# Performance work log

Hardware: AMD Instinct MI355X
Metric: run time of the kernel (lower is better)

## Reference

```python
import jax, jax.numpy as jnp
import numpy as np

B, S, D = 4, 1024, 1024
H = 16
DK = D // H  # per-head dim_q = dim_k = 64
DFF = 4096
EPS = 1e-5


def _layer_norm(x, g, b):
    m = jnp.mean(x, axis=-1, keepdims=True)
    v = jnp.mean((x - m) ** 2, axis=-1, keepdims=True)
    return (x - m) / jnp.sqrt(v + EPS) * g + b


def setup_inputs() -> dict:
    key = jax.random.key(0)
    ks = jax.random.split(key, 16)
    sd = 1.0 / np.sqrt(D)
    sk = 1.0 / np.sqrt(H * DK)
    sf = 1.0 / np.sqrt(DFF)
    return {
        "src": jax.random.normal(ks[0], (B, S, D), jnp.float32),
        # stacked per-head projections (torch loops over H separate nn.Linear)
        "Wq": jax.random.uniform(ks[1], (H, D, DK), jnp.float32, -sd, sd),
        "bq": jax.random.uniform(ks[2], (H, DK), jnp.float32, -sd, sd),
        "Wk": jax.random.uniform(ks[3], (H, D, DK), jnp.float32, -sd, sd),
        "bk": jax.random.uniform(ks[4], (H, DK), jnp.float32, -sd, sd),
        "Wv": jax.random.uniform(ks[5], (H, D, DK), jnp.float32, -sd, sd),
        "bv": jax.random.uniform(ks[6], (H, DK), jnp.float32, -sd, sd),
        "Wo": jax.random.uniform(ks[7], (H * DK, D), jnp.float32, -sk, sk),
        "bo": jax.random.uniform(ks[8], (D,), jnp.float32, -sk, sk),
        "g1": jnp.ones((D,), jnp.float32),
        "be1": jnp.zeros((D,), jnp.float32),
        "W1": jax.random.uniform(ks[9], (D, DFF), jnp.float32, -sd, sd),
        "b1": jax.random.uniform(ks[10], (DFF,), jnp.float32, -sd, sd),
        "W2": jax.random.uniform(ks[11], (DFF, D), jnp.float32, -sf, sf),
        "b2": jax.random.uniform(ks[12], (D,), jnp.float32, -sf, sf),
        "g2": jnp.ones((D,), jnp.float32),
        "be2": jnp.zeros((D,), jnp.float32),
    }


def reference(src, Wq, bq, Wk, bk, Wv, bv, Wo, bo, g1, be1, W1, b1, W2, b2, g2, be2):
    # multi-head attention (all heads batched via einsum instead of python loop)
    q = jnp.einsum("bsd,hdk->bhsk", src, Wq) + bq[None, :, None, :]
    k = jnp.einsum("bsd,hdk->bhsk", src, Wk) + bk[None, :, None, :]
    v = jnp.einsum("bsd,hdk->bhsk", src, Wv) + bv[None, :, None, :]
    scale = jnp.asarray(DK, src.dtype) ** 0.5  # query.size(-1) ** 0.5
    scores = jnp.einsum("bhsk,bhtk->bhst", q, k) / scale
    attn = jax.nn.softmax(scores, axis=-1)
    o = jnp.einsum("bhst,bhtk->bhsk", attn, v)  # [B,H,S,DK]
    o = o.transpose(0, 2, 1, 3).reshape(src.shape[0], src.shape[1], H * DK)
    attn_out = o @ Wo + bo
    x = _layer_norm(src + attn_out, g1, be1)
    ffn = jax.nn.relu(x @ W1 + b1) @ W2 + b2
    return _layer_norm(x + ffn, g2, be2)
```

## Files before the change

### kernel.cpp

```cpp
#include <hip/hip_runtime.h>
#include <hip/hip_bf16.h>

#define DEV __device__ __forceinline__

typedef __attribute__((ext_vector_type(8))) short bf16x8;
typedef __attribute__((ext_vector_type(4))) float f32x4;
typedef __attribute__((ext_vector_type(4))) short short4v;
typedef __attribute__((ext_vector_type(2))) unsigned uint2v;

DEV short f2bf(float f) {
    union { float f; unsigned u; } x; x.f = f;
    unsigned u = x.u;
    unsigned r = (u + 0x7fffu + ((u >> 16) & 1u)) >> 16;
    return (short)r;
}

DEV float bf2f(short s) {
    union { unsigned u; float f; } x;
    x.u = ((unsigned)(unsigned short)s) << 16;
    return x.f;
}

DEV unsigned cvtpk(float a, float b) {
    unsigned r;
    asm("v_cvt_pk_bf16_f32 %0, %1, %2" : "=v"(r) : "v"(a), "v"(b));
    return r;
}

#define GLD16(g, l)                                                         \
    __builtin_amdgcn_global_load_lds(                                       \
        (const __attribute__((address_space(1))) void*)(g),                 \
        (__attribute__((address_space(3))) void*)(l), 16, 0, 0)

#define WAITV(n) asm volatile("s_waitcnt vmcnt(" #n ")" ::: "memory")
#define SBAR()   asm volatile("s_barrier" ::: "memory")
#define LGKM0()                                              \
    asm volatile("s_waitcnt lgkmcnt(0)" ::: "memory");       \
    __builtin_amdgcn_sched_barrier(0)


__global__ __launch_bounds__(256) void k_cast(const float* __restrict__ in,
                                              short* __restrict__ out, int n4) {
    int i = blockIdx.x * 256 + threadIdx.x;
    if (i >= n4) return;
    float4 v = ((const float4*)in)[i];
    short4v o;
    o[0] = f2bf(v.x); o[1] = f2bf(v.y); o[2] = f2bf(v.z); o[3] = f2bf(v.w);
    ((short4v*)out)[i] = o;
}

__global__ __launch_bounds__(256) void k_tr(const float* __restrict__ in,
                                            short* __restrict__ out,
                                            int R, int C,
                                            long in_hs, long out_hs) {
    in  += (size_t)blockIdx.z * in_hs;
    out += (size_t)blockIdx.z * out_hs;
    __shared__ short tile[64][68];
    const int t = threadIdx.x;
    const int r0 = blockIdx.y * 64, c0 = blockIdx.x * 64;
    const int lr = t >> 4, lc4 = (t & 15) * 4;
#pragma unroll
    for (int it = 0; it < 4; ++it) {
        int r = lr + it * 16;
        float4 v = *(const float4*)(in + (size_t)(r0 + r) * C + c0 + lc4);
        tile[lc4 + 0][r] = f2bf(v.x);
        tile[lc4 + 1][r] = f2bf(v.y);
        tile[lc4 + 2][r] = f2bf(v.z);
        tile[lc4 + 3][r] = f2bf(v.w);
    }
    __syncthreads();
#pragma unroll
    for (int it = 0; it < 4; ++it) {
        int c = lr + it * 16;
        short4v o;
        o[0] = tile[c][lc4 + 0];
        o[1] = tile[c][lc4 + 1];
        o[2] = tile[c][lc4 + 2];
        o[3] = tile[c][lc4 + 3];
        *(short4v*)(out + (size_t)(c0 + c) * R + r0 + lc4) = o;
    }
}

template <int MODE>
__global__ __launch_bounds__(512, 2) void k_gemm8(
    const short* __restrict__ A, const short* __restrict__ BT,
    int K, int NT,
    const float* __restrict__ f0, const float* __restrict__ f1,
    const float* __restrict__ f2,
    void* __restrict__ o0, void* __restrict__ o1, void* __restrict__ o2) {
    __shared__ short lds[2][2][2][128 * 64];
    const int t = threadIdx.x;
    const int w = t >> 6, l = t & 63;
    const int l16 = l & 15, lg = l >> 4;
    const int wm = w >> 2, wn = w & 3;
    const int bn = blockIdx.x, bm = blockIdx.y;
    const int koff = blockIdx.z * NT * 64;
    const short* Ab = A + (size_t)bm * 256 * K + koff;
    const short* Bb = BT + (size_t)bn * 256 * K + koff;
    const int srow = l >> 3;
    const int scol = ((l & 7) ^ srow) * 8;
    const int offk0 = ((0 + lg) ^ (l16 & 7)) * 8;
    const int offk1 = ((4 + lg) ^ (l16 & 7)) * 8;

    f32x4 acc[8][4] = {};

    auto stg = [&](int buf, int op, int h, int kt) {
#pragma unroll
        for (int i = 0; i < 2; ++i) {
            int row = h * 128 + w * 16 + i * 8 + srow;
            GLD16((op ? Bb : Ab) + (size_t)row * K + (size_t)kt * 64 + scol,
                  &lds[buf][op][h][(w * 16 + i * 8) * 64]);
        }
    };

    stg(0, 0, 0, 0); stg(0, 0, 1, 0);
    stg(0, 1, 0, 0); stg(0, 1, 1, 0);
    const int t1p = (NT > 1) ? 1 : 0;
    stg(1, 1, 0, t1p); stg(1, 1, 1, t1p);
    WAITV(4);
    SBAR();

    for (int kt = 0; kt < NT; ++kt) {
        const int cur = kt & 1, nxt = cur ^ 1;
        const int t1 = (kt + 1 < NT) ? kt + 1 : NT - 1;
        const int t2 = (kt + 2 < NT) ? kt + 2 : NT - 1;
        bf16x8 a0[4][2], a1[4][2], b0[2][2], b1[2][2];

#pragma unroll
        for (int m = 0; m < 4; ++m) {
            a0[m][0] = *(const bf16x8*)&lds[cur][0][wm][(m * 16 + l16) * 64 + offk0];
            a0[m][1] = *(const bf16x8*)&lds[cur][0][wm][(m * 16 + l16) * 64 + offk1];
        }
#pragma unroll
        for (int n = 0; n < 2; ++n) {
            int r = (wn & 1) * 64 + n * 16 + l16;
            b0[n][0] = *(const bf16x8*)&lds[cur][1][wn >> 1][r * 64 + offk0];
            b0[n][1] = *(const bf16x8*)&lds[cur][1][wn >> 1][r * 64 + offk1];
        }
        stg(nxt, 0, 0, t1);
        SBAR();
        LGKM0();
        __builtin_amdgcn_s_setprio(1);
#pragma unroll
        for (int m = 0; m < 4; ++m)
#pragma unroll
            for (int n = 0; n < 2; ++n) {
                acc[m][n] = __builtin_amdgcn_mfma_f32_16x16x32_bf16(a0[m][0], b0[n][0], acc[m][n], 0, 0, 0);
                acc[m][n] = __builtin_amdgcn_mfma_f32_16x16x32_bf16(a0[m][1], b0[n][1], acc[m][n], 0, 0, 0);
            }
        __builtin_amdgcn_s_setprio(0);
        SBAR();

#pragma unroll
        for (int n = 0; n < 2; ++n) {
            int r = (wn & 1) * 64 + (n + 2) * 16 + l16;
            b1[n][0] = *(const bf16x8*)&lds[cur][1][wn >> 1][r * 64 + offk0];
            b1[n][1] = *(const bf16x8*)&lds[cur][1][wn >> 1][r * 64 + offk1];
        }
        stg(nxt, 0, 1, t1);
        SBAR();
        LGKM0();
        __builtin_amdgcn_s_setprio(1);
#pragma unroll
        for (int m = 0; m < 4; ++m)
#pragma unroll
            for (int n = 0; n < 2; ++n) {
                acc[m][n + 2] = __builtin_amdgcn_mfma_f32_16x16x32_bf16(a0[m][0], b1[n][0], acc[m][n + 2], 0, 0, 0);
                acc[m][n + 2] = __builtin_amdgcn_mfma_f32_16x16x32_bf16(a0[m][1], b1[n][1], acc[m][n + 2], 0, 0, 0);
            }
        __builtin_amdgcn_s_setprio(0);
        SBAR();

#pragma unroll
        for (int m = 0; m < 4; ++m) {
            a1[m][0] = *(const bf16x8*)&lds[cur][0][wm][((m + 4) * 16 + l16) * 64 + offk0];
            a1[m][1] = *(const bf16x8*)&lds[cur][0][wm][((m + 4) * 16 + l16) * 64 + offk1];
        }
        stg(cur, 1, 0, t2);
        SBAR();
        LGKM0();
        __builtin_amdgcn_s_setprio(1);
#pragma unroll
        for (int m = 0; m < 4; ++m)
#pragma unroll
            for (int n = 0; n < 2; ++n) {
                acc[m + 4][n + 2] = __builtin_amdgcn_mfma_f32_16x16x32_bf16(a1[m][0], b1[n][0], acc[m + 4][n + 2], 0, 0, 0);
                acc[m + 4][n + 2] = __builtin_amdgcn_mfma_f32_16x16x32_bf16(a1[m][1], b1[n][1], acc[m + 4][n + 2], 0, 0, 0);
            }
        __builtin_amdgcn_s_setprio(0);
        SBAR();

        stg(cur, 1, 1, t2);
        SBAR();
        __builtin_amdgcn_s_setprio(1);
#pragma unroll
        for (int m = 0; m < 4; ++m)
#pragma unroll
            for (int n = 0; n < 2; ++n) {
                acc[m + 4][n] = __builtin_amdgcn_mfma_f32_16x16x32_bf16(a1[m][0], b0[n][0], acc[m + 4][n], 0, 0, 0);
                acc[m + 4][n] = __builtin_amdgcn_mfma_f32_16x16x32_bf16(a1[m][1], b0[n][1], acc[m + 4][n], 0, 0, 0);
            }
        __builtin_amdgcn_s_setprio(0);
        WAITV(4);
        SBAR();
    }
    WAITV(0);

    const int N = gridDim.x * 256;
#pragma unroll
    for (int m = 0; m < 8; ++m) {
        int rowbase = bm * 256 + wm * 128 + m * 16 + lg * 4;
#pragma unroll
        for (int n = 0; n < 4; ++n) {
            int col = bn * 256 + wn * 64 + n * 16 + l16;
            if constexpr (MODE == 0) {
                int p = col >> 10, c1 = col & 1023;
                int hh = c1 >> 6, dk = c1 & 63;
                const float* bias = (p == 0) ? f0 : (p == 1) ? f1 : f2;
                float bvl = bias[c1];
                float qs = (p == 0) ? 0.18033688011112042f : 1.0f;
                int b = rowbase >> 10, s = rowbase & 1023;
                if (p == 2) {
                    short4v vv;
#pragma unroll
                    for (int rr = 0; rr < 4; ++rr) vv[rr] = f2bf(acc[m][n][rr] + bvl);
                    *(short4v*)((short*)o2 + (((size_t)(b * 16 + hh) * 64 + dk) << 10) + s) = vv;
                } else {
                    short* dst = (p == 0) ? (short*)o0 : (short*)o1;
#pragma unroll
                    for (int rr = 0; rr < 4; ++rr)
                        dst[(((size_t)(b * 16 + hh) << 10) + s + rr) * 64 + dk] =
                            f2bf((acc[m][n][rr] + bvl) * qs);
                }
            } else if constexpr (MODE == 2) {
                float bvl = f0[col];
#pragma unroll
                for (int rr = 0; rr < 4; ++rr) {
                    size_t idx = (size_t)(rowbase + rr) * N + col;
                    float y = acc[m][n][rr] + bvl;
                    ((short*)o0)[idx] = f2bf(y > 0.f ? y : 0.f);
                }
            } else {
                size_t base =
                    ((size_t)blockIdx.z * (gridDim.y * 256) + rowbase) * N + col;
#pragma unroll
                for (int rr = 0; rr < 4; ++rr)
                    ((short*)o0)[base + (size_t)rr * N] = f2bf(acc[m][n][rr]);
            }
        }
    }
}

__global__ __launch_bounds__(256) void k_gemm_s(
    const short* __restrict__ A, const short* __restrict__ BT, int K,
    const float* __restrict__ f0, const float* __restrict__ resid,
    float* __restrict__ o0) {
    __shared__ short Al[128][72];
    __shared__ short Bl[128][72];
    const int t = threadIdx.x;
    const int l = t & 63, w = t >> 6;
    const int l16 = l & 15, lg = l >> 4;
    const int wm = w >> 1, wn = w & 1;
    const int bn = blockIdx.x, bm = blockIdx.y;
    f32x4 acc[4][4] = {};
    const short* Ab = A + (size_t)bm * 128 * K;
    const short* Bb = BT + (size_t)bn * 128 * K;
    const int sr = t >> 3, sc = (t & 7) * 8;

    for (int k0 = 0; k0 < K; k0 += 64) {
#pragma unroll
        for (int it = 0; it < 4; ++it) {
            int rr = sr + it * 32;
            *(bf16x8*)&Al[rr][sc] = *(const bf16x8*)(Ab + (size_t)rr * K + k0 + sc);
            *(bf16x8*)&Bl[rr][sc] = *(const bf16x8*)(Bb + (size_t)rr * K + k0 + sc);
        }
        __syncthreads();
#pragma unroll
        for (int kk = 0; kk < 2; ++kk) {
            bf16x8 af[4], bfv[4];
#pragma unroll
            for (int i = 0; i < 4; ++i)
                af[i] = *(const bf16x8*)&Al[wm * 64 + i * 16 + l16][kk * 32 + lg * 8];
#pragma unroll
            for (int j = 0; j < 4; ++j)
                bfv[j] = *(const bf16x8*)&Bl[wn * 64 + j * 16 + l16][kk * 32 + lg * 8];
#pragma unroll
            for (int i = 0; i < 4; ++i)
#pragma unroll
                for (int j = 0; j < 4; ++j)
                    acc[i][j] = __builtin_amdgcn_mfma_f32_16x16x32_bf16(
                        af[i], bfv[j], acc[i][j], 0, 0, 0);
        }
        __syncthreads();
    }

    const int N = gridDim.x * 128;
#pragma unroll
    for (int i = 0; i < 4; ++i) {
#pragma unroll
        for (int rr = 0; rr < 4; ++rr) {
            int row = bm * 128 + wm * 64 + i * 16 + lg * 4 + rr;
#pragma unroll
            for (int j = 0; j < 4; ++j) {
                int col = bn * 128 + wn * 64 + j * 16 + l16;
                size_t idx = (size_t)row * N + col;
                o0[idx] = acc[i][j][rr] + f0[col] + resid[idx];
            }
        }
    }
}

__global__ __launch_bounds__(512, 4) void k_attn(const short* __restrict__ Q,
                                                 const short* __restrict__ Kt,
                                                 const short* __restrict__ VT,
                                                 short* __restrict__ O) {
    __shared__ short Kl[2][64 * 64];
    __shared__ short Vl[2][64 * 64];
    __shared__ short Pl[8][16 * 64];
    const int bh = blockIdx.x;
    const int qb = blockIdx.y;
    const int t = threadIdx.x;
    const int w = t >> 6, l = t & 63;
    const int l16 = l & 15, lg = l >> 4;
    const int sw = l16 & 7;
    const int pmask = (l16 & 7) << 1;
    const int srow = l >> 3;
    const int scol = ((l & 7) ^ srow) * 8;

    const short* Qb = Q + ((size_t)bh * 1024 + qb * 128 + w * 16 + l16) * 64 + lg * 8;
    bf16x8 qf0 = *(const bf16x8*)Qb;
    bf16x8 qf1 = *(const bf16x8*)(Qb + 32);

    const short* Kbase = Kt + (size_t)bh * (1024 * 64);
    const short* Vbase = VT + (size_t)bh * (64 * 1024);

    const float THR = 11.5415603f;

    bf16x8 ones;
#pragma unroll
    for (int i = 0; i < 8; ++i) ones[i] = (short)0x3F80;

    float m = -1e30f;
    f32x4 oacc[4] = {};
    f32x4 oaccS = {};

    auto stage = [&](int buf, int t0) {
        int roww = w * 8;
        GLD16(Kbase + (size_t)(t0 + roww + srow) * 64 + scol,
              &Kl[buf][roww * 64]);
        GLD16(Vbase + (size_t)(roww + srow) * 1024 + t0 + scol,
              &Vl[buf][roww * 64]);
    };

    auto compute = [&](int cur) {
        f32x4 s[4];
#pragma unroll
        for (int n = 0; n < 4; ++n) {
            bf16x8 kf0 = *(const bf16x8*)&Kl[cur][(n * 16 + l16) * 64 + (lg ^ sw) * 8];
            bf16x8 kf1 = *(const bf16x8*)&Kl[cur][(n * 16 + l16) * 64 + ((4 + lg) ^ sw) * 8];
            f32x4 a = {0.f, 0.f, 0.f, 0.f};
            a = __builtin_amdgcn_mfma_f32_16x16x32_bf16(kf0, qf0, a, 0, 0, 0);
            a = __builtin_amdgcn_mfma_f32_16x16x32_bf16(kf1, qf1, a, 0, 0, 0);
            s[n] = a;
        }
        float m1 = fmaxf(fmaxf(s[0][0], s[0][1]), s[0][2]);
        float m2 = fmaxf(fmaxf(s[0][3], s[1][0]), s[1][1]);
        float m3 = fmaxf(fmaxf(s[1][2], s[1][3]), s[2][0]);
        float m4 = fmaxf(fmaxf(s[2][1], s[2][2]), s[2][3]);
        float m5 = fmaxf(fmaxf(s[3][0], s[3][1]), s[3][2]);
        float mx = fmaxf(fmaxf(m1, m2), m3);
        mx = fmaxf(fmaxf(m4, m5), fmaxf(mx, s[3][3]));
        mx = fmaxf(mx, __shfl_xor(mx, 16));
        mx = fmaxf(mx, __shfl_xor(mx, 32));

        if (__any(mx > m + THR)) {
            float mn = fmaxf(m, mx);
            float al = exp2f(m - mn);
            m = mn;
#pragma unroll
            for (int n = 0; n < 4; ++n)
#pragma unroll
                for (int r = 0; r < 4; ++r) s[n][r] = exp2f(s[n][r] - m);
#pragma unroll
            for (int r = 0; r < 4; ++r) {
                float alr = __shfl(al, lg * 4 + r);
                oaccS[r] *= alr;
#pragma unroll
                for (int n = 0; n < 4; ++n) oacc[n][r] *= alr;
            }
        } else {
#pragma unroll
            for (int n = 0; n < 4; ++n)
#pragma unroll
                for (int r = 0; r < 4; ++r) s[n][r] = exp2f(s[n][r] - m);
        }
#pragma unroll
        for (int n = 0; n < 4; ++n) {
            uint2v pv;
            pv[0] = cvtpk(s[n][0], s[n][1]);
            pv[1] = cvtpk(s[n][2], s[n][3]);
            int g = (n * 4 + lg) ^ pmask;
            *(uint2v*)((char*)Pl[w] + l16 * 128 + g * 8) = pv;
        }
#pragma unroll
        for (int kk = 0; kk < 2; ++kk) {
            int gp = (8 * kk + 2 * lg) ^ pmask;
            bf16x8 pa = *(const bf16x8*)((const char*)Pl[w] + l16 * 128 + gp * 8);
            oaccS = __builtin_amdgcn_mfma_f32_16x16x32_bf16(pa, ones, oaccS, 0, 0, 0);
#pragma unroll
            for (int n = 0; n < 4; ++n) {
                bf16x8 vb = *(const bf16x8*)&Vl[cur][(n * 16 + l16) * 64 +
                                                     ((kk * 4 + lg) ^ sw) * 8];
                oacc[n] = __builtin_amdgcn_mfma_f32_16x16x32_bf16(pa, vb, oacc[n],
                                                                  0, 0, 0);
            }
        }
    };

    stage(0, 0);
    for (int ti = 0; ti < 15; ++ti) {
        int cur = ti & 1;
        stage(cur ^ 1, (ti + 1) * 64);
        WAITV(2);
        SBAR();
        compute(cur);
        SBAR();
    }
    WAITV(0);
    SBAR();
    compute(1);

    const int b = bh >> 4, h = bh & 15;
#pragma unroll
    for (int r = 0; r < 4; ++r) {
        float inv = 1.f / oaccS[r];
        size_t row = (size_t)(b * 1024 + qb * 128 + w * 16 + lg * 4 + r);
#pragma unroll
        for (int n = 0; n < 4; ++n)
            O[row * 1024 + h * 64 + n * 16 + l16] = f2bf(oacc[n][r] * inv);
    }
}

__global__ __launch_bounds__(256) void k_ln(const float* __restrict__ in,
                                            const float* __restrict__ g,
                                            const float* __restrict__ be,
                                            float* __restrict__ of,
                                            short* __restrict__ ob) {
    const int row = blockIdx.x, t = threadIdx.x;
    float4 x = ((const float4*)(in + ((size_t)row << 10)))[t];
    float s = x.x + x.y + x.z + x.w;
    float s2 = x.x * x.x + x.y * x.y + x.z * x.z + x.w * x.w;
#pragma unroll
    for (int mm = 1; mm < 64; mm <<= 1) {
        s += __shfl_xor(s, mm);
        s2 += __shfl_xor(s2, mm);
    }
    __shared__ float red[8];
    if ((t & 63) == 0) { red[t >> 6] = s; red[4 + (t >> 6)] = s2; }
    __syncthreads();
    s = red[0] + red[1] + red[2] + red[3];
    s2 = red[4] + red[5] + red[6] + red[7];
    float mean = s * (1.f / 1024.f);
    float var = s2 * (1.f / 1024.f) - mean * mean;
    float rstd = rsqrtf(var + 1e-5f);
    int c = t * 4;
    float4 y;
    y.x = (x.x - mean) * rstd * g[c + 0] + be[c + 0];
    y.y = (x.y - mean) * rstd * g[c + 1] + be[c + 1];
    y.z = (x.z - mean) * rstd * g[c + 2] + be[c + 2];
    y.w = (x.w - mean) * rstd * g[c + 3] + be[c + 3];
    if (of) ((float4*)(of + ((size_t)row << 10)))[t] = y;
    if (ob) {
        short4v o;
        o[0] = f2bf(y.x); o[1] = f2bf(y.y); o[2] = f2bf(y.z); o[3] = f2bf(y.w);
        ((short4v*)(ob + ((size_t)row << 10)))[t] = o;
    }
}

__global__ __launch_bounds__(256) void k_lnred(const short* __restrict__ part,
                                               const float* __restrict__ bias,
                                               const float* __restrict__ resid,
                                               const float* __restrict__ g,
                                               const float* __restrict__ be,
                                               float* __restrict__ of) {
    const int row = blockIdx.x, t = threadIdx.x;
    float4 x = ((const float4*)(resid + ((size_t)row << 10)))[t];
    float4 bv = ((const float4*)bias)[t];
    x.x += bv.x; x.y += bv.y; x.z += bv.z; x.w += bv.w;
#pragma unroll
    for (int kz = 0; kz < 4; ++kz) {
        short4v p = ((const short4v*)(part + (((size_t)kz * 4096 + row) << 10)))[t];
        x.x += bf2f(p[0]); x.y += bf2f(p[1]); x.z += bf2f(p[2]); x.w += bf2f(p[3]);
    }
    float s = x.x + x.y + x.z + x.w;
    float s2 = x.x * x.x + x.y * x.y + x.z * x.z + x.w * x.w;
#pragma unroll
    for (int mm = 1; mm < 64; mm <<= 1) {
        s += __shfl_xor(s, mm);
        s2 += __shfl_xor(s2, mm);
    }
    __shared__ float red[8];
    if ((t & 63) == 0) { red[t >> 6] = s; red[4 + (t >> 6)] = s2; }
    __syncthreads();
    s = red[0] + red[1] + red[2] + red[3];
    s2 = red[4] + red[5] + red[6] + red[7];
    float mean = s * (1.f / 1024.f);
    float var = s2 * (1.f / 1024.f) - mean * mean;
    float rstd = rsqrtf(var + 1e-5f);
    int c = t * 4;
    float4 y;
    y.x = (x.x - mean) * rstd * g[c + 0] + be[c + 0];
    y.y = (x.y - mean) * rstd * g[c + 1] + be[c + 1];
    y.z = (x.z - mean) * rstd * g[c + 2] + be[c + 2];
    y.w = (x.w - mean) * rstd * g[c + 3] + be[c + 3];
    ((float4*)(of + ((size_t)row << 10)))[t] = y;
}

extern "C" void kernel_launch(void* const* d_in, const int* in_sizes, int n_in,
                              void* d_out, int out_size, void* d_ws, size_t ws_size,
                              hipStream_t stream) {
    (void)in_sizes; (void)n_in; (void)out_size; (void)ws_size;
    const float* src = (const float*)d_in[0];
    const float* Wq  = (const float*)d_in[1];
    const float* bq  = (const float*)d_in[2];
    const float* Wk  = (const float*)d_in[3];
    const float* bk  = (const float*)d_in[4];
    const float* Wv  = (const float*)d_in[5];
    const float* bv  = (const float*)d_in[6];
    const float* Wo  = (const float*)d_in[7];
    const float* bo  = (const float*)d_in[8];
    const float* g1  = (const float*)d_in[9];
    const float* be1 = (const float*)d_in[10];
    const float* W1  = (const float*)d_in[11];
    const float* b1  = (const float*)d_in[12];
    const float* W2  = (const float*)d_in[13];
    const float* b2  = (const float*)d_in[14];
    const float* g2  = (const float*)d_in[15];
    const float* be2 = (const float*)d_in[16];

    char* ws = (char*)d_ws;
    const size_t MB = 1048576;
    short* srcbf = (short*)(ws + 0);
    short* Qb    = (short*)(ws + 8 * MB);
    short* Kb    = (short*)(ws + 16 * MB);
    short* VTb   = (short*)(ws + 24 * MB);
    short* h1    = (short*)(ws + 0);
    short* Obuf  = srcbf;
    short* W2T   = (short*)(ws + 32 * MB);
    float* xf    = (float*)(ws + 40 * MB);
    short* WqkvT = (short*)(ws + 56 * MB);
    short* WoT   = (short*)(ws + 62 * MB);
    short* W1T   = (short*)(ws + 64 * MB);
    float* xres  = (float*)(ws + 72 * MB);
    short* xbf   = (short*)(ws + 88 * MB);
    short* part  = (short*)(ws + 56 * MB);

    k_cast<<<4096, 256, 0, stream>>>(src, srcbf, 1048576);
    k_tr<<<dim3(1, 16, 16), 256, 0, stream>>>(Wq, WqkvT,           1024, 64, 65536, 65536);
    k_tr<<<dim3(1, 16, 16), 256, 0, stream>>>(Wk, WqkvT + 1048576, 1024, 64, 65536, 65536);
    k_tr<<<dim3(1, 16, 16), 256, 0, stream>>>(Wv, WqkvT + 2097152, 1024, 64, 65536, 65536);
    k_tr<<<dim3(16, 16, 1), 256, 0, stream>>>(Wo, WoT, 1024, 1024, 0, 0);
    k_tr<<<dim3(64, 16, 1), 256, 0, stream>>>(W1, W1T, 1024, 4096, 0, 0);
    k_tr<<<dim3(16, 64, 1), 256, 0, stream>>>(W2, W2T, 4096, 1024, 0, 0);
    k_gemm8<0><<<dim3(12, 16, 1), 512, 0, stream>>>(srcbf, WqkvT, 1024, 16,
                                                    bq, bk, bv, Qb, Kb, VTb);
    k_attn<<<dim3(64, 8), 512, 0, stream>>>(Qb, Kb, VTb, Obuf);
    k_gemm_s<<<dim3(8, 32), 256, 0, stream>>>(Obuf, WoT, 1024, bo, src, xres);
    k_ln<<<4096, 256, 0, stream>>>(xres, g1, be1, xf, xbf);
    k_gemm8<2><<<dim3(16, 16, 1), 512, 0, stream>>>(xbf, W1T, 1024, 16,
                                                    b1, nullptr, nullptr,
                                                    h1, nullptr, nullptr);
    k_gemm8<3><<<dim3(4, 16, 4), 512, 0, stream>>>(h1, W2T, 4096, 16,
                                                   nullptr, nullptr, nullptr,
                                                   part, nullptr, nullptr);
    k_lnred<<<4096, 256, 0, stream>>>(part, b2, xf, g2, be2, (float*)d_out);
}
```

Before: 214.7 us.

## Run Wo projection as split-K gemm8 and fuse partial reduction into LayerNorm

Replaces the simple 128x128 k_gemm_s output projection with the larger k_gemm8 kernel using 4-way split-K, writing bf16 partial sums to two buffers. The old standalone LayerNorm becomes k_lnwo, which sums the partials, bias and residual before normalizing. The goal is to use the faster MFMA gemm path and fill more CUs on the small output projection. The cost is extra partial-sum traffic and bf16 rounding of the partials, and the FFN2 partial-output addressing also changes.

```diff
diff --git a/kernel.cpp b/kernel.cpp
--- a/kernel.cpp
+++ b/kernel.cpp
@@ -241,70 +241,14 @@
                     ((short*)o0)[idx] = f2bf(y > 0.f ? y : 0.f);
                 }
             } else {
-                size_t base =
-                    ((size_t)blockIdx.z * (gridDim.y * 256) + rowbase) * N + col;
+                const int Mtot = gridDim.y * 256;
+                short* dst = (blockIdx.z < 3)
+                    ? (short*)o0 + (size_t)blockIdx.z * Mtot * N
+                    : (short*)o1;
+                size_t base = (size_t)rowbase * N + col;
 #pragma unroll
                 for (int rr = 0; rr < 4; ++rr)
-                    ((short*)o0)[base + (size_t)rr * N] = f2bf(acc[m][n][rr]);
-            }
-        }
-    }
-}
-
-__global__ __launch_bounds__(256) void k_gemm_s(
-    const short* __restrict__ A, const short* __restrict__ BT, int K,
-    const float* __restrict__ f0, const float* __restrict__ resid,
-    float* __restrict__ o0) {
-    __shared__ short Al[128][72];
-    __shared__ short Bl[128][72];
-    const int t = threadIdx.x;
-    const int l = t & 63, w = t >> 6;
-    const int l16 = l & 15, lg = l >> 4;
-    const int wm = w >> 1, wn = w & 1;
-    const int bn = blockIdx.x, bm = blockIdx.y;
-    f32x4 acc[4][4] = {};
-    const short* Ab = A + (size_t)bm * 128 * K;
-    const short* Bb = BT + (size_t)bn * 128 * K;
-    const int sr = t >> 3, sc = (t & 7) * 8;
-
-    for (int k0 = 0; k0 < K; k0 += 64) {
-#pragma unroll
-        for (int it = 0; it < 4; ++it) {
-            int rr = sr + it * 32;
-            *(bf16x8*)&Al[rr][sc] = *(const bf16x8*)(Ab + (size_t)rr * K + k0 + sc);
-            *(bf16x8*)&Bl[rr][sc] = *(const bf16x8*)(Bb + (size_t)rr * K + k0 + sc);
-        }
-        __syncthreads();
-#pragma unroll
-        for (int kk = 0; kk < 2; ++kk) {
-            bf16x8 af[4], bfv[4];
-#pragma unroll
-            for (int i = 0; i < 4; ++i)
-                af[i] = *(const bf16x8*)&Al[wm * 64 + i * 16 + l16][kk * 32 + lg * 8];
-#pragma unroll
-            for (int j = 0; j < 4; ++j)
-                bfv[j] = *(const bf16x8*)&Bl[wn * 64 + j * 16 + l16][kk * 32 + lg * 8];
-#pragma unroll
-            for (int i = 0; i < 4; ++i)
-#pragma unroll
-                for (int j = 0; j < 4; ++j)
-                    acc[i][j] = __builtin_amdgcn_mfma_f32_16x16x32_bf16(
-                        af[i], bfv[j], acc[i][j], 0, 0, 0);
-        }
-        __syncthreads();
-    }
-
-    const int N = gridDim.x * 128;
-#pragma unroll
-    for (int i = 0; i < 4; ++i) {
-#pragma unroll
-        for (int rr = 0; rr < 4; ++rr) {
-            int row = bm * 128 + wm * 64 + i * 16 + lg * 4 + rr;
-#pragma unroll
-            for (int j = 0; j < 4; ++j) {
-                int col = bn * 128 + wn * 64 + j * 16 + l16;
-                size_t idx = (size_t)row * N + col;
-                o0[idx] = acc[i][j][rr] + f0[col] + resid[idx];
+                    dst[base + (size_t)rr * N] = f2bf(acc[m][n][rr]);
             }
         }
     }
@@ -441,13 +385,27 @@
     }
 }
 
-__global__ __launch_bounds__(256) void k_ln(const float* __restrict__ in,
-                                            const float* __restrict__ g,
-                                            const float* __restrict__ be,
-                                            float* __restrict__ of,
-                                            short* __restrict__ ob) {
+__global__ __launch_bounds__(256) void k_lnwo(const short* __restrict__ p012,
+                                              const short* __restrict__ p3,
+                                              const float* __restrict__ bias,
+                                              const float* __restrict__ resid,
+                                              const float* __restrict__ g,
+                                              const float* __restrict__ be,
+                                              float* __restrict__ of,
+                                              short* __restrict__ ob) {
     const int row = blockIdx.x, t = threadIdx.x;
-    float4 x = ((const float4*)(in + ((size_t)row << 10)))[t];
+    float4 x = ((const float4*)(resid + ((size_t)row << 10)))[t];
+    float4 bv = ((const float4*)bias)[t];
+    x.x += bv.x; x.y += bv.y; x.z += bv.z; x.w += bv.w;
+#pragma unroll
+    for (int kz = 0; kz < 3; ++kz) {
+        short4v p = ((const short4v*)(p012 + (((size_t)kz * 4096 + row) << 10)))[t];
+        x.x += bf2f(p[0]); x.y += bf2f(p[1]); x.z += bf2f(p[2]); x.w += bf2f(p[3]);
+    }
+    {
+        short4v p = ((const short4v*)(p3 + ((size_t)row << 10)))[t];
+        x.x += bf2f(p[0]); x.y += bf2f(p[1]); x.z += bf2f(p[2]); x.w += bf2f(p[3]);
+    }
     float s = x.x + x.y + x.z + x.w;
     float s2 = x.x * x.x + x.y * x.y + x.z * x.z + x.w * x.w;
 #pragma unroll
@@ -469,12 +427,10 @@
     y.y = (x.y - mean) * rstd * g[c + 1] + be[c + 1];
     y.z = (x.z - mean) * rstd * g[c + 2] + be[c + 2];
     y.w = (x.w - mean) * rstd * g[c + 3] + be[c + 3];
-    if (of) ((float4*)(of + ((size_t)row << 10)))[t] = y;
-    if (ob) {
-        short4v o;
-        o[0] = f2bf(y.x); o[1] = f2bf(y.y); o[2] = f2bf(y.z); o[3] = f2bf(y.w);
-        ((short4v*)(ob + ((size_t)row << 10)))[t] = o;
-    }
+    ((float4*)(of + ((size_t)row << 10)))[t] = y;
+    short4v o;
+    o[0] = f2bf(y.x); o[1] = f2bf(y.y); o[2] = f2bf(y.z); o[3] = f2bf(y.w);
+    ((short4v*)(ob + ((size_t)row << 10)))[t] = o;
 }
 
 __global__ __launch_bounds__(256) void k_lnred(const short* __restrict__ part,
@@ -540,20 +496,21 @@
 
     char* ws = (char*)d_ws;
     const size_t MB = 1048576;
-    short* srcbf = (short*)(ws + 0);
-    short* Qb    = (short*)(ws + 8 * MB);
-    short* Kb    = (short*)(ws + 16 * MB);
-    short* VTb   = (short*)(ws + 24 * MB);
-    short* h1    = (short*)(ws + 0);
-    short* Obuf  = srcbf;
-    short* W2T   = (short*)(ws + 32 * MB);
-    float* xf    = (float*)(ws + 40 * MB);
-    short* WqkvT = (short*)(ws + 56 * MB);
-    short* WoT   = (short*)(ws + 62 * MB);
-    short* W1T   = (short*)(ws + 64 * MB);
-    float* xres  = (float*)(ws + 72 * MB);
-    short* xbf   = (short*)(ws + 88 * MB);
-    short* part  = (short*)(ws + 56 * MB);
+    short* srcbf  = (short*)(ws + 0);
+    short* Qb     = (short*)(ws + 8 * MB);
+    short* Kb     = (short*)(ws + 16 * MB);
+    short* VTb    = (short*)(ws + 24 * MB);
+    short* h1     = (short*)(ws + 0);
+    short* Obuf   = srcbf;
+    short* W2T    = (short*)(ws + 32 * MB);
+    float* xf     = (float*)(ws + 40 * MB);
+    short* WqkvT  = (short*)(ws + 56 * MB);
+    short* WoT    = (short*)(ws + 62 * MB);
+    short* W1T    = (short*)(ws + 64 * MB);
+    short* partWo0 = (short*)(ws + 8 * MB);
+    short* partWo3 = (short*)(ws + 72 * MB);
+    short* xbf    = (short*)(ws + 88 * MB);
+    short* part   = (short*)(ws + 56 * MB);
 
     k_cast<<<4096, 256, 0, stream>>>(src, srcbf, 1048576);
     k_tr<<<dim3(1, 16, 16), 256, 0, stream>>>(Wq, WqkvT,           1024, 64, 65536, 65536);
@@ -565,13 +522,16 @@
     k_gemm8<0><<<dim3(12, 16, 1), 512, 0, stream>>>(srcbf, WqkvT, 1024, 16,
                                                     bq, bk, bv, Qb, Kb, VTb);
     k_attn<<<dim3(64, 8), 512, 0, stream>>>(Qb, Kb, VTb, Obuf);
-    k_gemm_s<<<dim3(8, 32), 256, 0, stream>>>(Obuf, WoT, 1024, bo, src, xres);
-    k_ln<<<4096, 256, 0, stream>>>(xres, g1, be1, xf, xbf);
+    k_gemm8<3><<<dim3(4, 16, 4), 512, 0, stream>>>(Obuf, WoT, 1024, 4,
+                                                   nullptr, nullptr, nullptr,
+                                                   partWo0, partWo3, nullptr);
+    k_lnwo<<<4096, 256, 0, stream>>>(partWo0, partWo3, bo, src, g1, be1, xf, xbf);
     k_gemm8<2><<<dim3(16, 16, 1), 512, 0, stream>>>(xbf, W1T, 1024, 16,
                                                     b1, nullptr, nullptr,
                                                     h1, nullptr, nullptr);
     k_gemm8<3><<<dim3(4, 16, 4), 512, 0, stream>>>(h1, W2T, 4096, 16,
                                                    nullptr, nullptr, nullptr,
-                                                   part, nullptr, nullptr);
+                                                   part, part + 3u * 4194304u,
+                                                   nullptr);
     k_lnred<<<4096, 256, 0, stream>>>(part, b2, xf, g2, be2, (float*)d_out);
 }
```

Result: no change. 214.3 us (-0.2%).
